# Kernel tuning notes

Hardware: AMD Instinct MI355X
Metric: run time of the kernel (lower is better)

Reference implementation:

```python
import jax, jax.numpy as jnp
import numpy as np

NUM_LEVELS = 4
RADIUS = 4


def _bilinear_zeros(img, x, y):
    # img: (N, Hl, Wl); x, y: (N, K) pixel coords (align_corners=True identity map).
    # Replicates F.grid_sample(mode='bilinear', padding_mode='zeros', align_corners=True).
    N, Hl, Wl = img.shape
    x0 = jnp.floor(x); y0 = jnp.floor(y)
    wx1 = x - x0; wx0 = 1.0 - wx1
    wy1 = y - y0; wy0 = 1.0 - wy1
    bidx = jnp.arange(N)[:, None]

    def gather(xi, yi):
        inb = (xi >= 0) & (xi <= Wl - 1) & (yi >= 0) & (yi <= Hl - 1)
        xc = jnp.clip(xi, 0, Wl - 1).astype(jnp.int32)
        yc = jnp.clip(yi, 0, Hl - 1).astype(jnp.int32)
        vals = img[bidx, yc, xc]
        return jnp.where(inb, vals, jnp.zeros((), img.dtype))

    return (wy0 * wx0 * gather(x0, y0) + wy0 * wx1 * gather(x0 + 1, y0)
            + wy1 * wx0 * gather(x0, y0 + 1) + wy1 * wx1 * gather(x0 + 1, y0 + 1))


def setup_inputs() -> dict:
    key = jax.random.key(0)
    k1, k2, k3 = jax.random.split(key, 3)
    B, C, H, W = 2, 256, 64, 64
    fmap1 = jax.random.normal(k1, (B, C, H, W), dtype=jnp.float32)
    fmap2 = jax.random.normal(k2, (B, C, H, W), dtype=jnp.float32)
    # coords = base pixel grid + small random flow (stays mostly in-bounds)
    ys, xs = jnp.meshgrid(jnp.arange(H, dtype=jnp.float32), jnp.arange(W, dtype=jnp.float32), indexing='ij')
    grid = jnp.stack([xs, ys], axis=0)[None]  # (1, 2, H, W), channel0 = x
    flow = (jax.random.uniform(k3, (B, 2, H, W), dtype=jnp.float32) - 0.5) * 20.0
    coords = grid + flow
    return {'fmap1': fmap1, 'fmap2': fmap2, 'coords': coords}


def reference(fmap1, fmap2, coords):
    B, C, H, W = fmap1.shape
    HW = H * W
    # all-pairs correlation: (B, HW, HW), scaled by 1/sqrt(C)
    corr = jnp.einsum('bci,bcj->bij', fmap1.reshape(B, C, HW), fmap2.reshape(B, C, HW))
    corr = corr / jnp.sqrt(jnp.asarray(C, fmap1.dtype))
    corr = corr.reshape(B * HW, H, W)
    pyramid = [corr]
    for _ in range(NUM_LEVELS - 1):
        N, Hl, Wl = corr.shape
        corr = corr.reshape(N, Hl // 2, 2, Wl // 2, 2).mean(axis=(2, 4))  # avg_pool2d(2,2)
        pyramid.append(corr)

    r = RADIUS
    dy = jnp.linspace(-r, r, 2 * r + 1, dtype=coords.dtype)
    dx = jnp.linspace(-r, r, 2 * r + 1, dtype=coords.dtype)
    gy, gx = jnp.meshgrid(dy, dx, indexing='ij')  # matches torch.meshgrid(dy, dx)
    d0 = gy.reshape(-1); d1 = gx.reshape(-1)      # K = (2r+1)^2

    cperm = coords.transpose(0, 2, 3, 1).reshape(B * HW, 2)  # (N, 2), [:,0]=x, [:,1]=y
    outs = []
    for i, corr_l in enumerate(pyramid):
        cl = cperm / (2.0 ** i)
        # coords_lvl = centroid + delta; xgrid uses delta[...,0]=dy grid, ygrid uses delta[...,1]=dx grid
        x = cl[:, 0:1] + d0[None, :]
        y = cl[:, 1:2] + d1[None, :]
        outs.append(_bilinear_zeros(corr_l, x, y))  # (N, K)
    out = jnp.concatenate(outs, axis=-1)            # (N, num_levels*K)
    out = out.reshape(B, H, W, -1).transpose(0, 3, 1, 2)  # (B, 324, H, W)
    return out
```

## Files before the change

### kernel.cpp

```cpp
#include <hip/hip_runtime.h>
#include <cstdint>

#define B2 2
#define CCH 256
#define HH 64
#define WW 64
#define HWHW 4096
#define KOUT 324

typedef _Float16 half_t;
typedef _Float16 h2 __attribute__((ext_vector_type(2)));
typedef _Float16 h8 __attribute__((ext_vector_type(8)));
typedef float f32x4 __attribute__((ext_vector_type(4)));

#define P0 96
#define P1 64

__device__ __forceinline__ float fdot2f(h2 a, h2 b, float c) {
#if __has_builtin(__builtin_amdgcn_fdot2)
  return __builtin_amdgcn_fdot2(a, b, c, false);
#else
  return c + (float)a.x * (float)b.x + (float)a.y * (float)b.y;
#endif
}

__global__ __launch_bounds__(256) void zero_pads(float4* __restrict__ p, int n) {
  int i = blockIdx.x * 256 + threadIdx.x;
  if (i < n) p[i] = make_float4(0.f, 0.f, 0.f, 0.f);
}

__global__ __launch_bounds__(256) void transpose_cl(
    const float* __restrict__ f1, const float* __restrict__ f2,
    half_t* __restrict__ f1t, half_t* __restrict__ f2l0p) {
  __shared__ float tile[32][33];
  int zz = blockIdx.z;
  const float* src = (zz < 2) ? f1 : f2;
  float s = (zz < 2) ? 0.0625f : 1.0f;
  int b = zz & 1;
  int hw0 = blockIdx.x * 32;
  int c0 = blockIdx.y * 32;
  int tx = threadIdx.x;
  int ty = threadIdx.y;
  const float* sb = src + (size_t)b * CCH * HWHW;
#pragma unroll
  for (int i = 0; i < 4; i++)
    tile[ty + i * 8][tx] = sb[(size_t)(c0 + ty + i * 8) * HWHW + hw0 + tx];
  __syncthreads();
  if (zz < 2) {
    half_t* db = f1t + (size_t)b * HWHW * CCH;
#pragma unroll
    for (int i = 0; i < 4; i++)
      db[(size_t)(hw0 + ty + i * 8) * CCH + c0 + tx] = (half_t)(tile[tx][ty + i * 8] * s);
  } else {
    half_t* db = f2l0p + (size_t)b * P0 * P0 * CCH;
#pragma unroll
    for (int i = 0; i < 4; i++) {
      int hw = hw0 + ty + i * 8;
      int y = hw >> 6, x = hw & 63;
      db[(size_t)((y + 16) * P0 + (x + 16)) * CCH + c0 + tx] = (half_t)tile[tx][ty + i * 8];
    }
  }
}

__global__ __launch_bounds__(256) void pool_all(
    const h2* __restrict__ l0p, h2* __restrict__ l1p,
    h2* __restrict__ l2, h2* __restrict__ l3) {
  int idx = blockIdx.x * blockDim.x + threadIdx.x;
  const int n1 = B2 * 32 * 32 * 128;
  const int n2 = B2 * 16 * 16 * 128;
  const int n3 = B2 * 8 * 8 * 128;
  int L, Wo, local;
  if (idx < n1) { L = 1; Wo = 32; local = idx; }
  else if (idx < n1 + n2) { L = 2; Wo = 16; local = idx - n1; }
  else if (idx < n1 + n2 + n3) { L = 3; Wo = 8; local = idx - n1 - n2; }
  else return;
  int f = 1 << L;
  int sh = 6 - L;
  int c2 = local & 127;
  int t = local >> 7;
  int x = t & (Wo - 1);
  int y = (t >> sh) & (Wo - 1);
  int b = t >> (2 * sh);
  const h2* src = l0p + (size_t)b * P0 * P0 * 128 + c2;
  float ax = 0.f, ay = 0.f;
  for (int dy = 0; dy < f; dy++)
    for (int dx = 0; dx < f; dx++) {
      h2 a = src[(size_t)((y * f + dy + 16) * P0 + (x * f + dx + 16)) * 128];
      ax += (float)a.x; ay += (float)a.y;
    }
  float s = 1.0f / (float)(f * f);
  h2 r;
  r.x = (half_t)(ax * s);
  r.y = (half_t)(ay * s);
  if (L == 1)
    l1p[((size_t)b * P1 * P1 + (size_t)(y + 16) * P1 + (x + 16)) * 128 + c2] = r;
  else if (L == 2)
    l2[local] = r;
  else
    l3[local] = r;
}

__global__ __launch_bounds__(256) void corr23_k(
    const half_t* __restrict__ f1t,
    const half_t* __restrict__ f2l2, const half_t* __restrict__ f2l3,
    float* __restrict__ corr) {
  int bid = blockIdx.x;
  int g = ((bid & 7) << 6) | (bid >> 3);
  int n0 = g << 4;
  int b = n0 >> 12;
  int w = threadIdx.x >> 6;
  int l = threadIdx.x & 63;
  int row = l & 15;
  int kg = l >> 4;

  const h8* A = (const h8*)(f1t + ((size_t)(n0 + row) * CCH) + kg * 8);
  h8 a[8];
#pragma unroll
  for (int ks = 0; ks < 8; ks++) a[ks] = A[ks * 4];

  for (int nt = w * 5; nt < w * 5 + 5; nt++) {
    const half_t* Bb = (nt < 16)
        ? f2l2 + ((size_t)b * 256 + nt * 16) * CCH
        : f2l3 + ((size_t)b * 64 + (nt - 16) * 16) * CCH;
    const h8* Bp = (const h8*)(Bb + (size_t)row * CCH + kg * 8);
    f32x4 acc = {0.f, 0.f, 0.f, 0.f};
#pragma unroll
    for (int ks = 0; ks < 8; ks++)
      acc = __builtin_amdgcn_mfma_f32_16x16x32_f16(a[ks], Bp[ks * 4], acc, 0, 0, 0);
#pragma unroll
    for (int r = 0; r < 4; r++) {
      int q = kg * 4 + r;
      corr[(size_t)(n0 + q) * 320 + nt * 16 + row] = acc[r];
    }
  }
}

__device__ __forceinline__ float dpp_sum16(float x) {
  int v;
  v = __builtin_amdgcn_update_dpp(0, __float_as_int(x), 0xB1, 0xF, 0xF, true);
  x += __int_as_float(v);
  v = __builtin_amdgcn_update_dpp(0, __float_as_int(x), 0x4E, 0xF, 0xF, true);
  x += __int_as_float(v);
  v = __builtin_amdgcn_update_dpp(0, __float_as_int(x), 0x141, 0xF, 0xF, true);
  x += __int_as_float(v);
  v = __builtin_amdgcn_update_dpp(0, __float_as_int(x), 0x140, 0xF, 0xF, true);
  x += __int_as_float(v);
  return x;
}

__global__ __launch_bounds__(512, 8) void sample8(
    const float* __restrict__ coords,
    const half_t* __restrict__ f1t,
    const half_t* __restrict__ f2l0p, const half_t* __restrict__ f2l1p,
    const float* __restrict__ corr,
    float* __restrict__ out) {
  __shared__ float4 f1s4[256];
  __shared__ float P[2][8][100];
  __shared__ float wgt[2][8][4];
  __shared__ float cxy[2][8];

  int bid = blockIdx.x;
  int g = ((bid & 7) << 7) | (bid >> 3);
  int n0 = g << 3;
  int b = n0 >> 12;
  int i0 = n0 & 4095;
  int yi = i0 >> 6;
  int x0 = i0 & 63;
  int tid = threadIdx.x;

  if (tid < 256) f1s4[tid] = ((const float4*)(f1t + (size_t)n0 * CCH))[tid];
  if (tid < 16) {
    int q = tid & 7, c = tid >> 3;
    cxy[c][q] = coords[(size_t)(b * 2 + c) * HWHW + i0 + q];
  }
  __syncthreads();

  int w = tid >> 6;
  int l = w >> 2;
  int p = w & 3;
  int lane = tid & 63;
  int lg = lane >> 4;
  int l16 = lane & 15;

  int Pl = (l == 0) ? P0 : P1;
  float inv = (l == 0) ? 1.0f : 0.5f;
  const float4* f2b = (l == 0)
      ? (const float4*)f2l0p + ((size_t)b * P0 * P0 + 16 * P0 + 16) * 32 + l16
      : (const float4*)f2l1p + ((size_t)b * P1 * P1 + 16 * P1 + 16) * 32 + l16;
  const h2* f1h = (const h2*)f1s4;

  int q0 = 2 * p, q1 = 2 * p + 1;
  float xl0 = cxy[0][q0] * inv, yl0 = cxy[1][q0] * inv;
  float xl1 = cxy[0][q1] * inv, yl1 = cxy[1][q1] * inv;
  float fx0 = floorf(xl0), fy0 = floorf(yl0);
  float fx1 = floorf(xl1), fy1 = floorf(yl1);
  int ix00 = (int)fx0 - 4, iy00 = (int)fy0 - 4;
  int ix01 = (int)fx1 - 4, iy01 = (int)fy1 - 4;
  if (lane == 0) {
    wgt[l][q0][0] = 1.0f - (xl0 - fx0); wgt[l][q0][1] = xl0 - fx0;
    wgt[l][q0][2] = 1.0f - (yl0 - fy0); wgt[l][q0][3] = yl0 - fy0;
    wgt[l][q1][0] = 1.0f - (xl1 - fx1); wgt[l][q1][1] = xl1 - fx1;
    wgt[l][q1][2] = 1.0f - (yl1 - fy1); wgt[l][q1][3] = yl1 - fy1;
  }

  int fi0 = q0 * 128 + l16 * 4;
  h2 a00 = f1h[fi0], a01 = f1h[fi0 + 1], a02 = f1h[fi0 + 2], a03 = f1h[fi0 + 3];
  h2 a04 = f1h[fi0 + 64], a05 = f1h[fi0 + 65], a06 = f1h[fi0 + 66], a07 = f1h[fi0 + 67];
  int fi1 = q1 * 128 + l16 * 4;
  h2 a10 = f1h[fi1], a11 = f1h[fi1 + 1], a12 = f1h[fi1 + 2], a13 = f1h[fi1 + 3];
  h2 a14 = f1h[fi1 + 64], a15 = f1h[fi1 + 65], a16 = f1h[fi1 + 66], a17 = f1h[fi1 + 67];

  int v = lg, t = lg;
  int off0 = (iy00 + lg) * Pl + ix00;
  int off1 = (iy01 + lg) * Pl + ix01;
  const int dP = 4 * Pl;
  const int dW = 1 - 10 * Pl;
  for (int it = 0; it < 25; it++) {
    const float4* tp0 = f2b + (ptrdiff_t)off0 * 32;
    const float4* tp1 = f2b + (ptrdiff_t)off1 * 32;
    float4 A0 = tp0[0];
    float4 B0 = tp0[16];
    float4 A1 = tp1[0];
    float4 B1 = tp1[16];
    const h2* ah0 = (const h2*)&A0;
    const h2* bh0 = (const h2*)&B0;
    const h2* ah1 = (const h2*)&A1;
    const h2* bh1 = (const h2*)&B1;
    float d0 = 0.f, d1 = 0.f;
    d0 = fdot2f(ah0[0], a00, d0); d0 = fdot2f(ah0[1], a01, d0);
    d0 = fdot2f(ah0[2], a02, d0); d0 = fdot2f(ah0[3], a03, d0);
    d0 = fdot2f(bh0[0], a04, d0); d0 = fdot2f(bh0[1], a05, d0);
    d0 = fdot2f(bh0[2], a06, d0); d0 = fdot2f(bh0[3], a07, d0);
    d1 = fdot2f(ah1[0], a10, d1); d1 = fdot2f(ah1[1], a11, d1);
    d1 = fdot2f(ah1[2], a12, d1); d1 = fdot2f(ah1[3], a13, d1);
    d1 = fdot2f(bh1[0], a14, d1); d1 = fdot2f(bh1[1], a15, d1);
    d1 = fdot2f(bh1[2], a16, d1); d1 = fdot2f(bh1[3], a17, d1);
    d0 = dpp_sum16(d0);
    d1 = dpp_sum16(d1);
    if (l16 == 0) { P[l][q0][t] = d0; P[l][q1][t] = d1; }
    t += 4; v += 4;
    off0 += dP; off1 += dP;
    if (v >= 10) { v -= 10; off0 += dW; off1 += dW; }
  }
  __syncthreads();

#pragma unroll
  for (int it = 0; it < 3; it++) {
    int kidx = it * 64 + (tid >> 3);
    if (kidx < 162) {
      int lvl = kidx >= 81;
      int k = kidx - 81 * lvl;
      int q = tid & 7;
      int a = k / 9, bb2 = k - a * 9;
      float wx0 = wgt[lvl][q][0], wx1 = wgt[lvl][q][1];
      float wy0 = wgt[lvl][q][2], wy1 = wgt[lvl][q][3];
      const float* Pq = P[lvl][q];
      float val = wy0 * (wx0 * Pq[a * 10 + bb2] + wx1 * Pq[(a + 1) * 10 + bb2])
                + wy1 * (wx0 * Pq[a * 10 + bb2 + 1] + wx1 * Pq[(a + 1) * 10 + bb2 + 1]);
      out[(size_t)(b * KOUT + lvl * 81 + k) * HWHW + (size_t)yi * WW + x0 + q] = val;
    }
  }

#pragma unroll
  for (int it = 0; it < 3; it++) {
    int kidx = it * 64 + (tid >> 3);
    if (kidx < 162) {
      int lvl = 2 + (kidx >= 81);
      int k = kidx - 81 * (kidx >= 81);
      int q = tid & 7;
      float inv2 = (lvl == 2) ? 0.25f : 0.125f;
      int Wl2 = (lvl == 2) ? 16 : 8;
      int base = (lvl == 2) ? 0 : 256;
      float xl = cxy[0][q] * inv2, yl = cxy[1][q] * inv2;
      float fx = floorf(xl), fy = floorf(yl);
      int ix0 = (int)fx - 4, iy0 = (int)fy - 4;
      float wx1 = xl - fx, wx0 = 1.0f - wx1;
      float wy1 = yl - fy, wy0 = 1.0f - wy1;
      const float* cq = corr + (size_t)(n0 + q) * 320 + base;
      int a = k / 9, bb2 = k - a * 9;
      float p00 = 0.f, p10 = 0.f, p01 = 0.f, p11 = 0.f;
      {
        int x = ix0 + a, y = iy0 + bb2;
        if (((unsigned)x < (unsigned)Wl2) & ((unsigned)y < (unsigned)Wl2)) p00 = cq[y * Wl2 + x];
      }
      {
        int x = ix0 + a + 1, y = iy0 + bb2;
        if (((unsigned)x < (unsigned)Wl2) & ((unsigned)y < (unsigned)Wl2)) p10 = cq[y * Wl2 + x];
      }
      {
        int x = ix0 + a, y = iy0 + bb2 + 1;
        if (((unsigned)x < (unsigned)Wl2) & ((unsigned)y < (unsigned)Wl2)) p01 = cq[y * Wl2 + x];
      }
      {
        int x = ix0 + a + 1, y = iy0 + bb2 + 1;
        if (((unsigned)x < (unsigned)Wl2) & ((unsigned)y < (unsigned)Wl2)) p11 = cq[y * Wl2 + x];
      }
      float val = wy0 * (wx0 * p00 + wx1 * p10) + wy1 * (wx0 * p01 + wx1 * p11);
      out[(size_t)(b * KOUT + lvl * 81 + k) * HWHW + (size_t)yi * WW + x0 + q] = val;
    }
  }
}

extern "C" void kernel_launch(void* const* d_in, const int* in_sizes, int n_in,
                              void* d_out, int out_size, void* d_ws, size_t ws_size,
                              hipStream_t stream) {
  const float* fmap1 = (const float*)d_in[0];
  const float* fmap2 = (const float*)d_in[1];
  const float* coords = (const float*)d_in[2];
  float* out = (float*)d_out;

  char* ws = (char*)d_ws;
  half_t* f1t   = (half_t*)(ws);
  half_t* f2l0p = (half_t*)(ws + 4194304);
  half_t* f2l1p = (half_t*)(ws + 13631488);
  half_t* f2l2  = (half_t*)(ws + 17825792);
  half_t* f2l3  = (half_t*)(ws + 18087936);
  float*  corr  = (float*)(ws + 18153472);

  int nz = 13631488 / 16;
  zero_pads<<<nz / 256, 256, 0, stream>>>((float4*)f2l0p, nz);

  dim3 tb(32, 8, 1);
  dim3 tg(HWHW / 32, CCH / 32, 4);
  transpose_cl<<<tg, tb, 0, stream>>>(fmap1, fmap2, f1t, f2l0p);

  int npool = B2 * (32 * 32 + 16 * 16 + 8 * 8) * 128;
  pool_all<<<(npool + 255) / 256, 256, 0, stream>>>(
      (const h2*)f2l0p, (h2*)f2l1p, (h2*)f2l2, (h2*)f2l3);

  corr23_k<<<512, 256, 0, stream>>>(f1t, f2l2, f2l3, corr);

  sample8<<<1024, 512, 0, stream>>>(coords, f1t, f2l0p, f2l1p, corr, out);
}
```

Baseline: 145.4 us.

## Zero only padding borders inside transpose kernel; split sample loop per query

```diff
diff --git a/kernel.cpp b/kernel.cpp
--- a/kernel.cpp
+++ b/kernel.cpp
@@ -24,16 +24,45 @@
 #endif
 }
 
-__global__ __launch_bounds__(256) void zero_pads(float4* __restrict__ p, int n) {
-  int i = blockIdx.x * 256 + threadIdx.x;
-  if (i < n) p[i] = make_float4(0.f, 0.f, 0.f, 0.f);
-}
-
 __global__ __launch_bounds__(256) void transpose_cl(
     const float* __restrict__ f1, const float* __restrict__ f2,
-    half_t* __restrict__ f1t, half_t* __restrict__ f2l0p) {
+    half_t* __restrict__ f1t, half_t* __restrict__ f2l0p,
+    half_t* __restrict__ f2l1p) {
+  int zz = blockIdx.z;
+  if (zz == 4) {
+    const float4 zero = make_float4(0.f, 0.f, 0.f, 0.f);
+    int pb = blockIdx.y * 128 + blockIdx.x;
+    int t = threadIdx.y * 32 + threadIdx.x;
+#pragma unroll
+    for (int rep = 0; rep < 2; rep++) {
+      int f4 = t + rep * 256;
+      int pxi = f4 >> 5;
+      int c = f4 & 31;
+      if (pb < 640) {
+        int b = pb / 320, r = pb - b * 320;
+        int e = r * 16 + pxi;
+        int y, x;
+        if (e < 1536)      { y = e / 96; x = e - y * 96; }
+        else if (e < 3072) { int e2 = e - 1536; int yy = e2 / 96; y = 80 + yy; x = e2 - yy * 96; }
+        else if (e < 4096) { int e2 = e - 3072; y = 16 + (e2 >> 4); x = e2 & 15; }
+        else               { int e2 = e - 4096; y = 16 + (e2 >> 4); x = 80 + (e2 & 15); }
+        ((float4*)f2l0p)[((size_t)b * P0 * P0 + y * P0 + x) * 32 + c] = zero;
+      } else {
+        int pb2 = pb - 640;
+        int b = pb2 / 192, r = pb2 - b * 192;
+        int e = r * 16 + pxi;
+        int y, x;
+        if (e < 1024)      { y = e >> 6; x = e & 63; }
+        else if (e < 2048) { int e2 = e - 1024; y = 48 + (e2 >> 6); x = e2 & 63; }
+        else if (e < 2560) { int e2 = e - 2048; y = 16 + (e2 >> 4); x = e2 & 15; }
+        else               { int e2 = e - 2560; y = 16 + (e2 >> 4); x = 48 + (e2 & 15); }
+        ((float4*)f2l1p)[((size_t)b * P1 * P1 + y * P1 + x) * 32 + c] = zero;
+      }
+    }
+    return;
+  }
+
   __shared__ float tile[32][33];
-  int zz = blockIdx.z;
   const float* src = (zz < 2) ? f1 : f2;
   float s = (zz < 2) ? 0.0625f : 1.0f;
   int b = zz & 1;
@@ -188,59 +217,41 @@
       ? (const float4*)f2l0p + ((size_t)b * P0 * P0 + 16 * P0 + 16) * 32 + l16
       : (const float4*)f2l1p + ((size_t)b * P1 * P1 + 16 * P1 + 16) * 32 + l16;
   const h2* f1h = (const h2*)f1s4;
-
-  int q0 = 2 * p, q1 = 2 * p + 1;
-  float xl0 = cxy[0][q0] * inv, yl0 = cxy[1][q0] * inv;
-  float xl1 = cxy[0][q1] * inv, yl1 = cxy[1][q1] * inv;
-  float fx0 = floorf(xl0), fy0 = floorf(yl0);
-  float fx1 = floorf(xl1), fy1 = floorf(yl1);
-  int ix00 = (int)fx0 - 4, iy00 = (int)fy0 - 4;
-  int ix01 = (int)fx1 - 4, iy01 = (int)fy1 - 4;
-  if (lane == 0) {
-    wgt[l][q0][0] = 1.0f - (xl0 - fx0); wgt[l][q0][1] = xl0 - fx0;
-    wgt[l][q0][2] = 1.0f - (yl0 - fy0); wgt[l][q0][3] = yl0 - fy0;
-    wgt[l][q1][0] = 1.0f - (xl1 - fx1); wgt[l][q1][1] = xl1 - fx1;
-    wgt[l][q1][2] = 1.0f - (yl1 - fy1); wgt[l][q1][3] = yl1 - fy1;
-  }
-
-  int fi0 = q0 * 128 + l16 * 4;
-  h2 a00 = f1h[fi0], a01 = f1h[fi0 + 1], a02 = f1h[fi0 + 2], a03 = f1h[fi0 + 3];
-  h2 a04 = f1h[fi0 + 64], a05 = f1h[fi0 + 65], a06 = f1h[fi0 + 66], a07 = f1h[fi0 + 67];
-  int fi1 = q1 * 128 + l16 * 4;
-  h2 a10 = f1h[fi1], a11 = f1h[fi1 + 1], a12 = f1h[fi1 + 2], a13 = f1h[fi1 + 3];
-  h2 a14 = f1h[fi1 + 64], a15 = f1h[fi1 + 65], a16 = f1h[fi1 + 66], a17 = f1h[fi1 + 67];
-
-  int v = lg, t = lg;
-  int off0 = (iy00 + lg) * Pl + ix00;
-  int off1 = (iy01 + lg) * Pl + ix01;
   const int dP = 4 * Pl;
   const int dW = 1 - 10 * Pl;
-  for (int it = 0; it < 25; it++) {
-    const float4* tp0 = f2b + (ptrdiff_t)off0 * 32;
-    const float4* tp1 = f2b + (ptrdiff_t)off1 * 32;
-    float4 A0 = tp0[0];
-    float4 B0 = tp0[16];
-    float4 A1 = tp1[0];
-    float4 B1 = tp1[16];
-    const h2* ah0 = (const h2*)&A0;
-    const h2* bh0 = (const h2*)&B0;
-    const h2* ah1 = (const h2*)&A1;
-    const h2* bh1 = (const h2*)&B1;
-    float d0 = 0.f, d1 = 0.f;
-    d0 = fdot2f(ah0[0], a00, d0); d0 = fdot2f(ah0[1], a01, d0);
-    d0 = fdot2f(ah0[2], a02, d0); d0 = fdot2f(ah0[3], a03, d0);
-    d0 = fdot2f(bh0[0], a04, d0); d0 = fdot2f(bh0[1], a05, d0);
-    d0 = fdot2f(bh0[2], a06, d0); d0 = fdot2f(bh0[3], a07, d0);
-    d1 = fdot2f(ah1[0], a10, d1); d1 = fdot2f(ah1[1], a11, d1);
-    d1 = fdot2f(ah1[2], a12, d1); d1 = fdot2f(ah1[3], a13, d1);
-    d1 = fdot2f(bh1[0], a14, d1); d1 = fdot2f(bh1[1], a15, d1);
-    d1 = fdot2f(bh1[2], a16, d1); d1 = fdot2f(bh1[3], a17, d1);
-    d0 = dpp_sum16(d0);
-    d1 = dpp_sum16(d1);
-    if (l16 == 0) { P[l][q0][t] = d0; P[l][q1][t] = d1; }
-    t += 4; v += 4;
-    off0 += dP; off1 += dP;
-    if (v >= 10) { v -= 10; off0 += dW; off1 += dW; }
+
+  for (int qq = 0; qq < 2; qq++) {
+    int q = 2 * p + qq;
+    float xl = cxy[0][q] * inv, yl = cxy[1][q] * inv;
+    float fx = floorf(xl), fy = floorf(yl);
+    int ix0 = (int)fx - 4, iy0 = (int)fy - 4;
+    if (lane == 0) {
+      wgt[l][q][0] = 1.0f - (xl - fx); wgt[l][q][1] = xl - fx;
+      wgt[l][q][2] = 1.0f - (yl - fy); wgt[l][q][3] = yl - fy;
+    }
+    int fi = q * 128 + l16 * 4;
+    h2 a0 = f1h[fi + 0], a1 = f1h[fi + 1], a2 = f1h[fi + 2], a3 = f1h[fi + 3];
+    h2 a4 = f1h[fi + 64], a5 = f1h[fi + 65], a6 = f1h[fi + 66], a7 = f1h[fi + 67];
+
+    int v = lg, t = lg;
+    int off = (iy0 + lg) * Pl + ix0;
+    for (int it = 0; it < 25; it++) {
+      const float4* tp = f2b + (ptrdiff_t)off * 32;
+      float4 A = tp[0];
+      float4 Bv = tp[16];
+      const h2* ah = (const h2*)&A;
+      const h2* bh = (const h2*)&Bv;
+      float d = 0.f;
+      d = fdot2f(ah[0], a0, d); d = fdot2f(ah[1], a1, d);
+      d = fdot2f(ah[2], a2, d); d = fdot2f(ah[3], a3, d);
+      d = fdot2f(bh[0], a4, d); d = fdot2f(bh[1], a5, d);
+      d = fdot2f(bh[2], a6, d); d = fdot2f(bh[3], a7, d);
+      d = dpp_sum16(d);
+      if (l16 == 0) P[l][q][t] = d;
+      t += 4; v += 4;
+      off += dP;
+      if (v >= 10) { v -= 10; off += dW; }
+    }
   }
   __syncthreads();
 
@@ -317,12 +328,9 @@
   half_t* f2l3  = (half_t*)(ws + 18087936);
   float*  corr  = (float*)(ws + 18153472);
 
-  int nz = 13631488 / 16;
-  zero_pads<<<nz / 256, 256, 0, stream>>>((float4*)f2l0p, nz);
-
   dim3 tb(32, 8, 1);
-  dim3 tg(HWHW / 32, CCH / 32, 4);
-  transpose_cl<<<tg, tb, 0, stream>>>(fmap1, fmap2, f1t, f2l0p);
+  dim3 tg(HWHW / 32, CCH / 32, 5);
+  transpose_cl<<<tg, tb, 0, stream>>>(fmap1, fmap2, f1t, f2l0p, f2l1p);
 
   int npool = B2 * (32 * 32 + 16 * 16 + 8 * 8) * 128;
   pool_all<<<(npool + 255) / 256, 256, 0, stream>>>(
```

Result: no change. 145.6 us (+0.1%).
